# Optimization experiments

Hardware: AMD Instinct MI355X
Metric: run time of the kernel (lower is better)

Reference implementation:

```python
import jax, jax.numpy as jnp
import numpy as np

FS = 256  # sampling_rate
BANDS = [(0.5, 45.0), (0.5, 4.0), (4.0, 8.0), (8.0, 13.0), (13.0, 30.0), (30.0, 45.0)]
EPS = 1e-8


def _bandpass(sig, lo, hi):
    # FFT-domain brick-wall bandpass, matching bandpass_filter_fft
    T = sig.shape[-1]
    F = jnp.fft.rfft(sig, axis=-1)
    freqs = np.fft.rfftfreq(T, d=1.0 / FS)
    mask = jnp.asarray(((freqs >= lo) & (freqs <= hi)).astype(np.float32))
    return jnp.fft.irfft(F * mask, n=T, axis=-1)


def _phase(sig):
    # Hilbert transform -> instantaneous phase
    T = sig.shape[-1]
    h = np.zeros(T, np.float32)
    if T % 2 == 0:
        h[0] = 1.0; h[T // 2] = 1.0; h[1:T // 2] = 2.0
    else:
        h[0] = 1.0; h[1:(T + 1) // 2] = 2.0
    analytic = jnp.fft.ifft(jnp.fft.fft(sig, axis=-1) * jnp.asarray(h), axis=-1)
    return jnp.angle(analytic)


def _zscore(x):
    # matches torch: (x - mean) / (std_unbiased + 1e-8)
    m = x.mean(-1, keepdims=True)
    s = jnp.std(x, axis=-1, keepdims=True, ddof=1)
    return (x - m) / (s + EPS)


def _band_feats(e1, e2, lo, hi):
    B, C, T = e1.shape
    f1 = _bandpass(e1, lo, hi)
    f2 = _bandpass(e2, lo, hi)
    p1 = f1 ** 2
    p2 = f2 ** 2
    ph1 = _phase(f1)
    ph2 = _phase(f2)

    # PLV = |mean_t exp(i(phi1_i - phi2_j))| -> complex matmul over T
    z1 = jnp.exp(1j * ph1)                       # (B,C,T) complex64
    z2c = jnp.exp(-1j * ph2)
    plv = jnp.abs(jnp.einsum('bit,bjt->bij', z1, z2c)) / T

    # pairwise phase differences (B,C,C,T) -- honors the original full CxC structure
    pd = ph1[:, :, None, :] - ph2[:, None, :, :]
    s = jnp.sign(pd)
    pli = jnp.abs(s.mean(-1))

    # wPLI: power-weighted sign, weights normalized over T per (i,j)
    w = (p1[:, :, None, :] + p2[:, None, :, :]) * 0.5
    wn = w / (w.sum(-1, keepdims=True) + EPS)
    wpli = jnp.abs((s * wn).sum(-1))

    # Coherence: |X_i Y_j*|^2 / (|X_i|^2 |Y_j|^2 + eps), mean over freqs
    X1 = jnp.fft.rfft(f1, axis=-1)
    X2 = jnp.fft.rfft(f2, axis=-1)
    P1 = jnp.abs(X1) ** 2                        # (B,C,F)
    P2 = jnp.abs(X2) ** 2
    pw = P1[:, :, None, :] * P2[:, None, :, :]   # == |pxy|^2 == pxx*pyy
    coh = (pw / (pw + EPS)).mean(-1)

    # Power correlation: z-score over T then matmul / T
    pz1 = _zscore(p1)
    pz2 = _zscore(p2)
    pcorr = jnp.einsum('bit,bjt->bij', pz1, pz2) / T

    # Phase difference magnitude
    phdiff = jnp.abs(pd).mean(-1)

    # Time-domain correlation
    tz1 = _zscore(f1)
    tz2 = _zscore(f2)
    tcorr = jnp.einsum('bit,bjt->bij', tz1, tz2) / T

    # feature order: PLV, PLI, wPLI, Coherence, Power_Corr, Phase_Diff, Time_Corr
    return jnp.stack([plv, pli, wpli, coh, pcorr, phdiff, tcorr], axis=1)  # (B,7,C,C)


def setup_inputs() -> dict:
    key = jax.random.key(0)
    k1, k2 = jax.random.split(key)
    eeg1 = jax.random.normal(k1, (4, 64, 2048), dtype=jnp.float32)
    eeg2 = jax.random.normal(k2, (4, 64, 2048), dtype=jnp.float32)
    return {"eeg1": eeg1, "eeg2": eeg2}


def reference(eeg1, eeg2):
    # feature_type='all' -> all 7 features, 6 bands -> (B, 6, 7, C, C)
    feats = [_band_feats(eeg1, eeg2, lo, hi) for lo, hi in BANDS]
    return jnp.stack(feats, axis=1)
```

## Files before the change

### kernel.cpp

```cpp
#include <hip/hip_runtime.h>
#include <math.h>

__constant__ int c_klo[6] = {4, 4, 32, 64, 104, 240};
__constant__ int c_nk[6]  = {357, 29, 33, 41, 137, 121};

#define PI2_N 0.0030679615757712823f

__global__ __launch_bounds__(256) void k_dft(const float* __restrict__ e1,
                                             const float* __restrict__ e2,
                                             float2* __restrict__ coef,
                                             float* __restrict__ pwr) {
  __shared__ float xs[2048];
  __shared__ float red[4][64][2];
  int sig = blockIdx.x;
  int b = sig >> 7, side = (sig >> 6) & 1, ch = sig & 63;
  int bside = b * 2 + side;
  const float* src = (side ? e2 : e1) + (size_t)(b * 64 + ch) * 2048;
  for (int q = 0; q < 2; ++q) {
    int i4 = q * 256 + threadIdx.x;
    ((float4*)xs)[i4] = ((const float4*)src)[i4];
  }
  __syncthreads();
  int binlane = threadIdx.x & 63, tch = threadIdx.x >> 6;
  int t0 = tch << 9;
  const float* xp = xs + t0;
  for (int rnd = 0; rnd < 6; ++rnd) {
    int kidx = rnd * 64 + binlane;
    int k = kidx + 4;
    float wr, wi, sr, si;
    sincosf(-(float)((k * t0) & 2047) * PI2_N, &wi, &wr);
    sincosf(-(float)k * PI2_N, &si, &sr);
    float are = 0.f, aim = 0.f;
    for (int tt = 0; tt < 512; tt += 4) {
      float4 xv = *(const float4*)(xp + tt);
      float nr, ni;
      are = fmaf(xv.x, wr, are); aim = fmaf(xv.x, wi, aim);
      nr = fmaf(wr, sr, -(wi * si)); ni = fmaf(wr, si, wi * sr); wr = nr; wi = ni;
      are = fmaf(xv.y, wr, are); aim = fmaf(xv.y, wi, aim);
      nr = fmaf(wr, sr, -(wi * si)); ni = fmaf(wr, si, wi * sr); wr = nr; wi = ni;
      are = fmaf(xv.z, wr, are); aim = fmaf(xv.z, wi, aim);
      nr = fmaf(wr, sr, -(wi * si)); ni = fmaf(wr, si, wi * sr); wr = nr; wi = ni;
      are = fmaf(xv.w, wr, are); aim = fmaf(xv.w, wi, aim);
      nr = fmaf(wr, sr, -(wi * si)); ni = fmaf(wr, si, wi * sr); wr = nr; wi = ni;
    }
    red[tch][binlane][0] = are;
    red[tch][binlane][1] = aim;
    __syncthreads();
    if (tch == 0 && kidx < 357) {
      float rr = red[0][binlane][0] + red[1][binlane][0] + red[2][binlane][0] + red[3][binlane][0];
      float ri = red[0][binlane][1] + red[1][binlane][1] + red[2][binlane][1] + red[3][binlane][1];
      int a = (bside * 357 + kidx) * 64 + ch;
      coef[a] = make_float2(rr, ri);
      pwr[a] = rr * rr + ri * ri;
    }
    __syncthreads();
  }
}

__global__ __launch_bounds__(256) void k_analytic(const float* __restrict__ coef,
                                                  float* __restrict__ fields) {
  __shared__ float Lt[2][64][65];
  int tchunk = blockIdx.x, bside = blockIdx.y, split = blockIdx.z;
  int lane = threadIdx.x & 63;
  int ch0 = (threadIdx.x >> 6) << 4;
  int t = tchunk * 64 + lane;
  float Rr, Ri; sincosf((float)t * PI2_N, &Ri, &Rr);
  int k0 = (split == 0) ? 4 : (split == 1 ? 104 : 240);
  float Wr, Wi; { int m = (k0 * t) & 2047; sincosf((float)m * PI2_N, &Wi, &Wr); }
  float ar[16], ai[16];
#pragma unroll
  for (int c = 0; c < 16; ++c) { ar[c] = 0.f; ai[c] = 0.f; }
  const float* cb = coef + (size_t)(bside * 357 + (k0 - 4)) * 128 + ch0 * 2;
  int kk = 0;

  auto accum = [&](int n) {
    int e = kk + n;
#pragma unroll 2
    for (; kk < e; ++kk) {
      const float* F = cb + (size_t)kk * 128;
#pragma unroll
      for (int q = 0; q < 8; ++q) {
        float4 Fv = *(const float4*)(F + q * 4);
        ar[2 * q]     = fmaf(Fv.x, Wr, ar[2 * q]);     ar[2 * q]     = fmaf(-Fv.y, Wi, ar[2 * q]);
        ai[2 * q]     = fmaf(Fv.x, Wi, ai[2 * q]);     ai[2 * q]     = fmaf( Fv.y, Wr, ai[2 * q]);
        ar[2 * q + 1] = fmaf(Fv.z, Wr, ar[2 * q + 1]); ar[2 * q + 1] = fmaf(-Fv.w, Wi, ar[2 * q + 1]);
        ai[2 * q + 1] = fmaf(Fv.z, Wi, ai[2 * q + 1]); ai[2 * q + 1] = fmaf( Fv.w, Wr, ai[2 * q + 1]);
      }
      float nr = fmaf(Wr, Rr, -(Wi * Ri));
      float ni = fmaf(Wr, Ri, Wi * Rr);
      Wr = nr; Wi = ni;
    }
  };

  auto emitBand = [&](int band) {
#pragma unroll
    for (int c = 0; c < 16; ++c) {
      Lt[0][ch0 + c][lane] = ar[c] * (1.f / 1024.f);
      Lt[1][ch0 + c][lane] = ai[c] * (1.f / 1024.f);
    }
    __syncthreads();
    size_t base = (size_t)((band * 8 + bside) * 2) * 131072 + (size_t)tchunk * 4096;
    for (int idx = threadIdx.x; idx < 2048; idx += 256) {
      int fi = idx >> 10, r = idx & 1023, tt = r >> 4, c4 = (r & 15) * 4;
      float4 v = make_float4(Lt[fi][c4][tt], Lt[fi][c4 + 1][tt], Lt[fi][c4 + 2][tt], Lt[fi][c4 + 3][tt]);
      *(float4*)(fields + base + (size_t)fi * 131072 + tt * 64 + c4) = v;
    }
    __syncthreads();
#pragma unroll
    for (int c = 0; c < 16; ++c) { ar[c] = 0.f; ai[c] = 0.f; }
  };

  auto stepback = [&]() {
    float nr = fmaf(Wr, Rr, Wi * Ri);
    float ni = fmaf(Wi, Rr, -(Wr * Ri));
    Wr = nr; Wi = ni; kk -= 1;
  };

  if (split == 0) {
    accum(29); emitBand(1); stepback();
    accum(33); emitBand(2); stepback();
    accum(41); emitBand(3);
  } else if (split == 1) {
    accum(137); emitBand(4);
  } else {
    accum(121); emitBand(5);
  }
}

__global__ __launch_bounds__(256) void k_band0(const float* __restrict__ fields_in,
                                               const float* __restrict__ coef,
                                               float* __restrict__ fields) {
  int idx = blockIdx.x * 256 + threadIdx.x;
  int ch = idx & 63, t = (idx >> 6) & 2047, bsd = idx >> 17;
  size_t o = (size_t)t * 64 + ch;
  float re = 0.f, im = 0.f;
#pragma unroll
  for (int b = 1; b <= 5; ++b) {
    re += fields_in[(size_t)((b * 8 + bsd) * 2 + 0) * 131072 + o];
    im += fields_in[(size_t)((b * 8 + bsd) * 2 + 1) * 131072 + o];
  }
  const int dk[4] = {32, 64, 104, 240};
#pragma unroll
  for (int q = 0; q < 4; ++q) {
    int k = dk[q];
    const float* F = coef + ((size_t)(bsd * 357 + (k - 4)) * 64 + ch) * 2;
    float fx = F[0], fy = F[1];
    float s, c; sincosf((float)((k * t) & 2047) * PI2_N, &s, &c);
    re -= (fx * c - fy * s) * (1.f / 1024.f);
    im -= (fx * s + fy * c) * (1.f / 1024.f);
  }
  fields[(size_t)(bsd * 2 + 0) * 131072 + o] = re;
  fields[(size_t)(bsd * 2 + 1) * 131072 + o] = im;
}

__global__ __launch_bounds__(256, 2) void k_pairs(const float* __restrict__ fields,
                                                  float* __restrict__ part,
                                                  float* __restrict__ sqp) {
  __shared__ float le[2][4][16][64];
  int ts = blockIdx.x, bb = blockIdx.y;
  int band = bb >> 2, b = bb & 3;
  int tid = threadIdx.x;
  int ti = tid >> 4, tj = tid & 15;
  const float* bi = fields + (size_t)((band * 8 + b * 2 + 0) * 2) * 131072;
  const float* bj = fields + (size_t)((band * 8 + b * 2 + 1) * 2) * 131072;
  float acc[7][4][4];
#pragma unroll
  for (int a = 0; a < 7; ++a)
#pragma unroll
    for (int il = 0; il < 4; ++il)
#pragma unroll
      for (int jl = 0; jl < 4; ++jl) acc[a][il][jl] = 0.f;
  float sqa = 0.f;
  int lside = tid >> 7, lr = tid & 127, ltt = lr >> 3, lc8 = (lr & 7) * 8;
  const float* lbase = lside ? bj : bi;
  int sside = (tid >> 6) & 1, sch = tid & 63, shalf = tid >> 7;
  int tb = ts * 128;
  for (int sub = 0; sub < 8; ++sub) {
    int t0 = tb + sub * 16;
    {
      const float* rp = lbase + (size_t)(t0 + ltt) * 64 + lc8;
      float4 reA = *(const float4*)rp;
      float4 reB = *(const float4*)(rp + 4);
      float4 imA = *(const float4*)(rp + 131072);
      float4 imB = *(const float4*)(rp + 131072 + 4);
      float re8[8] = {reA.x, reA.y, reA.z, reA.w, reB.x, reB.y, reB.z, reB.w};
      float im8[8] = {imA.x, imA.y, imA.z, imA.w, imB.x, imB.y, imB.z, imB.w};
#pragma unroll
      for (int e = 0; e < 8; ++e) {
        float re = re8[e], im = im8[e];
        float mag2 = fmaf(re, re, im * im);
        float rinv = mag2 > 0.f ? rsqrtf(mag2) : 0.f;
        float cc = mag2 > 0.f ? re * rinv : 1.f;
        float ss = im * rinv;
        float ph = atan2f(im, re);
        le[lside][0][ltt][lc8 + e] = ph;
        le[lside][1][ltt][lc8 + e] = cc;
        le[lside][2][ltt][lc8 + e] = ss;
        le[lside][3][ltt][lc8 + e] = re;
      }
    }
    __syncthreads();
#pragma unroll
    for (int u = 0; u < 8; ++u) {
      float v = le[sside][3][shalf * 8 + u][sch];
      float p = v * v;
      sqa = fmaf(p, p, sqa);
    }
#pragma unroll 2
    for (int tt = 0; tt < 16; ++tt) {
      float4 vph1 = *(const float4*)&le[0][0][tt][ti * 4];
      float4 vc1 = *(const float4*)&le[0][1][tt][ti * 4];
      float4 vs1 = *(const float4*)&le[0][2][tt][ti * 4];
      float4 vf1 = *(const float4*)&le[0][3][tt][ti * 4];
      float4 vph2 = *(const float4*)&le[1][0][tt][tj * 4];
      float4 vc2 = *(const float4*)&le[1][1][tt][tj * 4];
      float4 vs2 = *(const float4*)&le[1][2][tt][tj * 4];
      float4 vf2 = *(const float4*)&le[1][3][tt][tj * 4];
      float ph1a[4] = {vph1.x, vph1.y, vph1.z, vph1.w};
      float c1a[4] = {vc1.x, vc1.y, vc1.z, vc1.w};
      float s1a[4] = {vs1.x, vs1.y, vs1.z, vs1.w};
      float f1a[4] = {vf1.x, vf1.y, vf1.z, vf1.w};
      float ph2a[4] = {vph2.x, vph2.y, vph2.z, vph2.w};
      float c2a[4] = {vc2.x, vc2.y, vc2.z, vc2.w};
      float s2a[4] = {vs2.x, vs2.y, vs2.z, vs2.w};
      float f2a[4] = {vf2.x, vf2.y, vf2.z, vf2.w};
      float p1a[4] = {f1a[0] * f1a[0], f1a[1] * f1a[1], f1a[2] * f1a[2], f1a[3] * f1a[3]};
      float p2a[4] = {f2a[0] * f2a[0], f2a[1] * f2a[1], f2a[2] * f2a[2], f2a[3] * f2a[3]};
#pragma unroll
      for (int il = 0; il < 4; ++il) {
#pragma unroll
        for (int jl = 0; jl < 4; ++jl) {
          float pd = ph1a[il] - ph2a[jl];
          float sg = pd > 0.f ? 1.f : -1.f;
          acc[2][il][jl] += sg;
          acc[3][il][jl] = fmaf(sg, p1a[il], acc[3][il][jl]);
          acc[4][il][jl] = fmaf(sg, p2a[jl], acc[4][il][jl]);
          acc[5][il][jl] += fabsf(pd);
          acc[0][il][jl] = fmaf(c1a[il], c2a[jl], acc[0][il][jl]);
          acc[0][il][jl] = fmaf(s1a[il], s2a[jl], acc[0][il][jl]);
          acc[1][il][jl] = fmaf(s1a[il], c2a[jl], acc[1][il][jl]);
          acc[1][il][jl] = fmaf(-c1a[il], s2a[jl], acc[1][il][jl]);
          acc[6][il][jl] = fmaf(p1a[il], p2a[jl], acc[6][il][jl]);
        }
      }
    }
    __syncthreads();
  }
  int pb = (bb * 16 + ts) * 7;
#pragma unroll
  for (int a = 0; a < 7; ++a)
#pragma unroll
    for (int il = 0; il < 4; ++il) {
      int ro = (ti * 4 + il) * 64 + tj * 4;
      *(float4*)&part[(size_t)(pb + a) * 4096 + ro] =
          make_float4(acc[a][il][0], acc[a][il][1], acc[a][il][2], acc[a][il][3]);
    }
  ((float*)le)[tid] = sqa;
  __syncthreads();
  if (tid < 128) {
    sqp[(size_t)(bb * 16 + ts) * 128 + tid] = ((float*)le)[tid] + ((float*)le)[tid + 128];
  }
}

__global__ __launch_bounds__(256) void k_stats(const float* __restrict__ pwr,
                                               const float* __restrict__ sqp,
                                               float* __restrict__ stats) {
  int gid = blockIdx.x * 256 + threadIdx.x;
  int band = gid >> 9, bsd = (gid >> 6) & 7, ch = gid & 63;
  int b = bsd >> 1, side = bsd & 1;
  int kl = c_klo[band] - 4, nk = c_nk[band];
  const float* pp = pwr + (size_t)(bsd * 357 + kl) * 64 + ch;
  float sp = 0.f;
  for (int kkq = 0; kkq < nk; ++kkq) sp += pp[kkq * 64];
  sp *= (1.f / 1024.f);
  int bb = band * 4 + b;
  const float* qp = sqp + (size_t)(bb * 16) * 128 + side * 64 + ch;
  float sq = 0.f;
#pragma unroll 4
  for (int tsq = 0; tsq < 16; ++tsq) sq += qp[tsq * 128];
  stats[gid * 2] = sp;
  stats[gid * 2 + 1] = sq;
}

__global__ __launch_bounds__(256) void k_final(const float* __restrict__ part,
                                               const float* __restrict__ stats,
                                               const float* __restrict__ pwr,
                                               const float* __restrict__ coef,
                                               float* __restrict__ out) {
  int gid = blockIdx.x * 256 + threadIdx.x;
  int bb = gid >> 12, rem = gid & 4095;
  int band = bb >> 2, b = bb & 3;
  int i = rem >> 6, j = rem & 63;
  float S[7];
#pragma unroll
  for (int a = 0; a < 7; ++a) S[a] = 0.f;
  const float* pp = part + (size_t)bb * 16 * 7 * 4096 + rem;
  for (int ts = 0; ts < 16; ++ts)
#pragma unroll
    for (int a = 0; a < 7; ++a) S[a] += pp[(ts * 7 + a) * 4096];
  const float* st1 = stats + (size_t)((band * 8 + b * 2 + 0) * 64 + i) * 2;
  const float* st2 = stats + (size_t)((band * 8 + b * 2 + 1) * 64 + j) * 2;
  float sp1 = st1[0], sq1 = st1[1];
  float sp2 = st2[0], sq2 = st2[1];
  const float T = 2048.f, Ti = 1.f / 2048.f, Vi = 1.f / 2047.f;
  float plv = sqrtf(S[0] * S[0] + S[1] * S[1]) * Ti;
  float pli = fabsf(S[2]) * Ti;
  float wpli = fabsf(0.5f * (S[3] + S[4])) / (0.5f * (sp1 + sp2) + 1e-8f);
  int kl = c_klo[band] - 4, n = c_nk[band];
  const float* P1 = pwr + (size_t)((b * 2 + 0) * 357 + kl) * 64 + i;
  const float* P2 = pwr + (size_t)((b * 2 + 1) * 357 + kl) * 64 + j;
  const float* C1 = coef + ((size_t)((b * 2 + 0) * 357 + kl) * 64 + i) * 2;
  const float* C2 = coef + ((size_t)((b * 2 + 1) * 357 + kl) * 64 + j) * 2;
  float coh = 0.f, cross = 0.f;
  for (int kkq = 0; kkq < n; ++kkq) {
    float r = P1[kkq * 64] * P2[kkq * 64];
    coh += __fdividef(r, r + 1e-8f);
    float2 a = *(const float2*)(C1 + kkq * 128);
    float2 c = *(const float2*)(C2 + kkq * 128);
    cross = fmaf(a.x, c.x, fmaf(a.y, c.y, cross));
  }
  coh *= (1.f / 1025.f);
  float mp1 = sp1 * Ti, mp2 = sp2 * Ti;
  float sd1 = sqrtf(fmaxf((sq1 - T * mp1 * mp1) * Vi, 0.f));
  float sd2 = sqrtf(fmaxf((sq2 - T * mp2 * mp2) * Vi, 0.f));
  float pcorr = (S[6] - T * mp1 * mp2) / ((sd1 + 1e-8f) * (sd2 + 1e-8f)) * Ti;
  float phd = S[5] * Ti;
  float se1 = sqrtf(sp1 * Vi);
  float se2 = sqrtf(sp2 * Vi);
  float tcorr = (cross * (1.f / 1024.f)) / ((se1 + 1e-8f) * (se2 + 1e-8f)) * Ti;
  size_t ob = (size_t)((b * 6 + band) * 7) * 4096 + rem;
  out[ob] = plv;
  out[ob + 4096] = pli;
  out[ob + 2 * 4096] = wpli;
  out[ob + 3 * 4096] = coh;
  out[ob + 4 * 4096] = pcorr;
  out[ob + 5 * 4096] = phd;
  out[ob + 6 * 4096] = tcorr;
}

extern "C" void kernel_launch(void* const* d_in, const int* in_sizes, int n_in,
                              void* d_out, int out_size, void* d_ws, size_t ws_size,
                              hipStream_t stream) {
  const float* e1 = (const float*)d_in[0];
  const float* e2 = (const float*)d_in[1];
  float* out = (float*)d_out;
  char* ws = (char*)d_ws;
  size_t off = 0;
  auto alloc = [&](size_t bytes) -> void* {
    void* p = ws + off;
    off += (bytes + 255) & ~(size_t)255;
    return p;
  };
  float2* coef = (float2*)alloc((size_t)8 * 357 * 64 * 8);
  float* pwr = (float*)alloc((size_t)8 * 357 * 64 * 4);
  float* fields = (float*)alloc((size_t)6 * 8 * 2 * 131072 * 4);
  float* sqp = (float*)alloc((size_t)24 * 16 * 128 * 4);
  float* stats = (float*)alloc((size_t)6 * 8 * 64 * 2 * 4);
  float* part = (float*)alloc((size_t)24 * 16 * 7 * 4096 * 4);
  (void)in_sizes; (void)n_in; (void)out_size; (void)ws_size;

  hipLaunchKernelGGL(k_dft, dim3(512), dim3(256), 0, stream, e1, e2, coef, pwr);
  hipLaunchKernelGGL(k_analytic, dim3(32, 8, 3), dim3(256), 0, stream, (const float*)coef, fields);
  hipLaunchKernelGGL(k_band0, dim3(4096), dim3(256), 0, stream, fields, (const float*)coef, fields);
  hipLaunchKernelGGL(k_pairs, dim3(16, 24), dim3(256), 0, stream, fields, part, sqp);
  hipLaunchKernelGGL(k_stats, dim3(12), dim3(256), 0, stream, pwr, sqp, stats);
  hipLaunchKernelGGL(k_final, dim3(384), dim3(256), 0, stream, part, stats, pwr, (const float*)coef, out);
}
```

Before: 413.7 us.

## Stage DFT coefficients in LDS for analytic synthesis and move fourth-power sums to stats

k_analytic now copies chunks of 35 coefficient rows into shared memory and recomputes the twiddle start for each chunk and band. This replaces the per-thread global float4 loads and the stepback trick, and the kernel gets a launch bound of 2 blocks per CU. The sum-of-p^2 reduction is moved out of k_pairs into a rewritten k_stats that reads the fields directly. This frees k_pairs registers, and its occupancy hint is dropped, at the cost of an extra read of fields in k_stats.

```diff
diff --git a/kernel.cpp b/kernel.cpp
--- a/kernel.cpp
+++ b/kernel.cpp
@@ -57,42 +57,60 @@
   }
 }
 
-__global__ __launch_bounds__(256) void k_analytic(const float* __restrict__ coef,
-                                                  float* __restrict__ fields) {
+#define CS 35
+__global__ __launch_bounds__(256, 2) void k_analytic(const float* __restrict__ coef,
+                                                     float* __restrict__ fields) {
+  __shared__ float Fs[CS * 128];
   __shared__ float Lt[2][64][65];
   int tchunk = blockIdx.x, bside = blockIdx.y, split = blockIdx.z;
   int lane = threadIdx.x & 63;
   int ch0 = (threadIdx.x >> 6) << 4;
   int t = tchunk * 64 + lane;
   float Rr, Ri; sincosf((float)t * PI2_N, &Ri, &Rr);
-  int k0 = (split == 0) ? 4 : (split == 1 ? 104 : 240);
-  float Wr, Wi; { int m = (k0 * t) & 2047; sincosf((float)m * PI2_N, &Wi, &Wr); }
-  float ar[16], ai[16];
-#pragma unroll
-  for (int c = 0; c < 16; ++c) { ar[c] = 0.f; ai[c] = 0.f; }
-  const float* cb = coef + (size_t)(bside * 357 + (k0 - 4)) * 128 + ch0 * 2;
-  int kk = 0;
-
-  auto accum = [&](int n) {
-    int e = kk + n;
+  int bandList[3], ksList[3], nkList[3], nb;
+  if (split == 0) {
+    nb = 3;
+    bandList[0] = 1; ksList[0] = 4;  nkList[0] = 29;
+    bandList[1] = 2; ksList[1] = 32; nkList[1] = 33;
+    bandList[2] = 3; ksList[2] = 64; nkList[2] = 41;
+  } else if (split == 1) {
+    nb = 1; bandList[0] = 4; ksList[0] = 104; nkList[0] = 137;
+  } else {
+    nb = 1; bandList[0] = 5; ksList[0] = 240; nkList[0] = 121;
+  }
+  for (int bi = 0; bi < nb; ++bi) {
+    int band = bandList[bi], ks = ksList[bi], nk = nkList[bi];
+    float ar[16], ai[16];
+#pragma unroll
+    for (int c = 0; c < 16; ++c) { ar[c] = 0.f; ai[c] = 0.f; }
+    for (int c0 = 0; c0 < nk; c0 += CS) {
+      int kc = min(CS, nk - c0);
+      __syncthreads();
+      {
+        const float4* srcp = (const float4*)(coef + (size_t)(bside * 357 + (ks - 4) + c0) * 128);
+        for (int idx = threadIdx.x; idx < kc * 32; idx += 256)
+          ((float4*)Fs)[idx] = srcp[idx];
+      }
+      __syncthreads();
+      float Wr, Wi; { int m = ((ks + c0) * t) & 2047; sincosf((float)m * PI2_N, &Wi, &Wr); }
+      const float* Fb = Fs + ch0 * 2;
 #pragma unroll 2
-    for (; kk < e; ++kk) {
-      const float* F = cb + (size_t)kk * 128;
-#pragma unroll
-      for (int q = 0; q < 8; ++q) {
-        float4 Fv = *(const float4*)(F + q * 4);
-        ar[2 * q]     = fmaf(Fv.x, Wr, ar[2 * q]);     ar[2 * q]     = fmaf(-Fv.y, Wi, ar[2 * q]);
-        ai[2 * q]     = fmaf(Fv.x, Wi, ai[2 * q]);     ai[2 * q]     = fmaf( Fv.y, Wr, ai[2 * q]);
-        ar[2 * q + 1] = fmaf(Fv.z, Wr, ar[2 * q + 1]); ar[2 * q + 1] = fmaf(-Fv.w, Wi, ar[2 * q + 1]);
-        ai[2 * q + 1] = fmaf(Fv.z, Wi, ai[2 * q + 1]); ai[2 * q + 1] = fmaf( Fv.w, Wr, ai[2 * q + 1]);
+      for (int kk = 0; kk < kc; ++kk) {
+        const float* F = Fb + kk * 128;
+#pragma unroll
+        for (int q = 0; q < 8; ++q) {
+          float4 Fv = *(const float4*)(F + q * 4);
+          ar[2 * q]     = fmaf(Fv.x, Wr, ar[2 * q]);     ar[2 * q]     = fmaf(-Fv.y, Wi, ar[2 * q]);
+          ai[2 * q]     = fmaf(Fv.x, Wi, ai[2 * q]);     ai[2 * q]     = fmaf( Fv.y, Wr, ai[2 * q]);
+          ar[2 * q + 1] = fmaf(Fv.z, Wr, ar[2 * q + 1]); ar[2 * q + 1] = fmaf(-Fv.w, Wi, ar[2 * q + 1]);
+          ai[2 * q + 1] = fmaf(Fv.z, Wi, ai[2 * q + 1]); ai[2 * q + 1] = fmaf( Fv.w, Wr, ai[2 * q + 1]);
+        }
+        float nr = fmaf(Wr, Rr, -(Wi * Ri));
+        float ni = fmaf(Wr, Ri, Wi * Rr);
+        Wr = nr; Wi = ni;
       }
-      float nr = fmaf(Wr, Rr, -(Wi * Ri));
-      float ni = fmaf(Wr, Ri, Wi * Rr);
-      Wr = nr; Wi = ni;
-    }
-  };
-
-  auto emitBand = [&](int band) {
+    }
+    __syncthreads();
 #pragma unroll
     for (int c = 0; c < 16; ++c) {
       Lt[0][ch0 + c][lane] = ar[c] * (1.f / 1024.f);
@@ -105,25 +123,6 @@
       float4 v = make_float4(Lt[fi][c4][tt], Lt[fi][c4 + 1][tt], Lt[fi][c4 + 2][tt], Lt[fi][c4 + 3][tt]);
       *(float4*)(fields + base + (size_t)fi * 131072 + tt * 64 + c4) = v;
     }
-    __syncthreads();
-#pragma unroll
-    for (int c = 0; c < 16; ++c) { ar[c] = 0.f; ai[c] = 0.f; }
-  };
-
-  auto stepback = [&]() {
-    float nr = fmaf(Wr, Rr, Wi * Ri);
-    float ni = fmaf(Wi, Rr, -(Wr * Ri));
-    Wr = nr; Wi = ni; kk -= 1;
-  };
-
-  if (split == 0) {
-    accum(29); emitBand(1); stepback();
-    accum(33); emitBand(2); stepback();
-    accum(41); emitBand(3);
-  } else if (split == 1) {
-    accum(137); emitBand(4);
-  } else {
-    accum(121); emitBand(5);
   }
 }
 
@@ -153,9 +152,8 @@
   fields[(size_t)(bsd * 2 + 1) * 131072 + o] = im;
 }
 
-__global__ __launch_bounds__(256, 2) void k_pairs(const float* __restrict__ fields,
-                                                  float* __restrict__ part,
-                                                  float* __restrict__ sqp) {
+__global__ __launch_bounds__(256) void k_pairs(const float* __restrict__ fields,
+                                               float* __restrict__ part) {
   __shared__ float le[2][4][16][64];
   int ts = blockIdx.x, bb = blockIdx.y;
   int band = bb >> 2, b = bb & 3;
@@ -170,10 +168,8 @@
     for (int il = 0; il < 4; ++il)
 #pragma unroll
       for (int jl = 0; jl < 4; ++jl) acc[a][il][jl] = 0.f;
-  float sqa = 0.f;
   int lside = tid >> 7, lr = tid & 127, ltt = lr >> 3, lc8 = (lr & 7) * 8;
   const float* lbase = lside ? bj : bi;
-  int sside = (tid >> 6) & 1, sch = tid & 63, shalf = tid >> 7;
   int tb = ts * 128;
   for (int sub = 0; sub < 8; ++sub) {
     int t0 = tb + sub * 16;
@@ -200,12 +196,6 @@
       }
     }
     __syncthreads();
-#pragma unroll
-    for (int u = 0; u < 8; ++u) {
-      float v = le[sside][3][shalf * 8 + u][sch];
-      float p = v * v;
-      sqa = fmaf(p, p, sqa);
-    }
 #pragma unroll 2
     for (int tt = 0; tt < 16; ++tt) {
       float4 vph1 = *(const float4*)&le[0][0][tt][ti * 4];
@@ -255,31 +245,31 @@
       *(float4*)&part[(size_t)(pb + a) * 4096 + ro] =
           make_float4(acc[a][il][0], acc[a][il][1], acc[a][il][2], acc[a][il][3]);
     }
-  ((float*)le)[tid] = sqa;
+}
+
+__global__ __launch_bounds__(256) void k_stats(const float* __restrict__ fields,
+                                               const float* __restrict__ pwr,
+                                               float* __restrict__ stats) {
+  __shared__ float red[256];
+  int bb = blockIdx.x;
+  int band = bb >> 3, bsd = bb & 7;
+  int ch = threadIdx.x & 63, tq = threadIdx.x >> 6;
+  const float* fp = fields + (size_t)((band * 8 + bsd) * 2) * 131072 + (size_t)tq * 512 * 64 + ch;
+  float s4 = 0.f;
+  for (int tt = 0; tt < 512; ++tt) { float v = fp[tt * 64]; float p = v * v; s4 = fmaf(p, p, s4); }
+  red[threadIdx.x] = s4;
   __syncthreads();
-  if (tid < 128) {
-    sqp[(size_t)(bb * 16 + ts) * 128 + tid] = ((float*)le)[tid] + ((float*)le)[tid + 128];
-  }
-}
-
-__global__ __launch_bounds__(256) void k_stats(const float* __restrict__ pwr,
-                                               const float* __restrict__ sqp,
-                                               float* __restrict__ stats) {
-  int gid = blockIdx.x * 256 + threadIdx.x;
-  int band = gid >> 9, bsd = (gid >> 6) & 7, ch = gid & 63;
-  int b = bsd >> 1, side = bsd & 1;
-  int kl = c_klo[band] - 4, nk = c_nk[band];
-  const float* pp = pwr + (size_t)(bsd * 357 + kl) * 64 + ch;
-  float sp = 0.f;
-  for (int kkq = 0; kkq < nk; ++kkq) sp += pp[kkq * 64];
-  sp *= (1.f / 1024.f);
-  int bb = band * 4 + b;
-  const float* qp = sqp + (size_t)(bb * 16) * 128 + side * 64 + ch;
-  float sq = 0.f;
-#pragma unroll 4
-  for (int tsq = 0; tsq < 16; ++tsq) sq += qp[tsq * 128];
-  stats[gid * 2] = sp;
-  stats[gid * 2 + 1] = sq;
+  if (tq == 0) {
+    float sq = red[ch] + red[64 + ch] + red[128 + ch] + red[192 + ch];
+    int kl = c_klo[band] - 4, nk = c_nk[band];
+    const float* pp = pwr + (size_t)(bsd * 357 + kl) * 64 + ch;
+    float sp = 0.f;
+    for (int kkq = 0; kkq < nk; ++kkq) sp += pp[kkq * 64];
+    sp *= (1.f / 1024.f);
+    int o = ((band * 8 + bsd) * 64 + ch) * 2;
+    stats[o] = sp;
+    stats[o + 1] = sq;
+  }
 }
 
 __global__ __launch_bounds__(256) void k_final(const float* __restrict__ part,
@@ -354,7 +344,6 @@
   float2* coef = (float2*)alloc((size_t)8 * 357 * 64 * 8);
   float* pwr = (float*)alloc((size_t)8 * 357 * 64 * 4);
   float* fields = (float*)alloc((size_t)6 * 8 * 2 * 131072 * 4);
-  float* sqp = (float*)alloc((size_t)24 * 16 * 128 * 4);
   float* stats = (float*)alloc((size_t)6 * 8 * 64 * 2 * 4);
   float* part = (float*)alloc((size_t)24 * 16 * 7 * 4096 * 4);
   (void)in_sizes; (void)n_in; (void)out_size; (void)ws_size;
@@ -362,7 +351,7 @@
   hipLaunchKernelGGL(k_dft, dim3(512), dim3(256), 0, stream, e1, e2, coef, pwr);
   hipLaunchKernelGGL(k_analytic, dim3(32, 8, 3), dim3(256), 0, stream, (const float*)coef, fields);
   hipLaunchKernelGGL(k_band0, dim3(4096), dim3(256), 0, stream, fields, (const float*)coef, fields);
-  hipLaunchKernelGGL(k_pairs, dim3(16, 24), dim3(256), 0, stream, fields, part, sqp);
-  hipLaunchKernelGGL(k_stats, dim3(12), dim3(256), 0, stream, pwr, sqp, stats);
+  hipLaunchKernelGGL(k_pairs, dim3(16, 24), dim3(256), 0, stream, fields, part);
+  hipLaunchKernelGGL(k_stats, dim3(48), dim3(256), 0, stream, fields, pwr, stats);
   hipLaunchKernelGGL(k_final, dim3(384), dim3(256), 0, stream, part, stats, pwr, (const float*)coef, out);
 }
```

Result: faster. 348.2 us (-15.8%).
